# Kernel tuning notes

Measured on AMD Instinct MI355X. Metric: run time of the kernel, lower is better.

Reference implementation:

```python
import jax, jax.numpy as jnp
import numpy as np

N = 40000
E = 640000
F_IN = 128
F_OUT = 128


def setup_inputs() -> dict:
    key = jax.random.key(0)
    ks = jax.random.split(key, 8)
    x = jax.random.normal(ks[0], (N, F_IN), dtype=jnp.float32)
    weight = jax.random.normal(ks[1], (F_IN, F_OUT), dtype=jnp.float32) * (1.0 / np.sqrt(F_OUT))
    node_w = jax.random.normal(ks[2], (F_IN, 1), dtype=jnp.float32)
    sem_w = jax.random.normal(ks[3], (F_IN,), dtype=jnp.float32) * (1.0 / np.sqrt(F_IN))
    bias = jax.random.normal(ks[4], (F_OUT,), dtype=jnp.float32) * 0.01
    adj_val = jax.random.uniform(ks[5], (E,), dtype=jnp.float32)
    src = jax.random.randint(ks[6], (E,), 0, N, dtype=jnp.int32)
    dst = jax.random.randint(ks[7], (E,), 0, N, dtype=jnp.int32)
    return {"x": x, "weight": weight, "node_w": node_w, "sem_w": sem_w,
            "bias": bias, "adj_val": adj_val, "src": src, "dst": dst}


def reference(x, weight, node_w, sem_w, bias, adj_val, src, dst):
    # node-level attention: per-node sigmoid scalar [N, 1]
    node_att = jax.nn.sigmoid(x @ node_w)
    # semantic-level attention: softmax over feature weight vector [F_in]
    sem_att = jax.nn.softmax(sem_w)
    # hierarchical weighting, then dense projection [N, F_out]
    support = (x * node_att * sem_att) @ weight
    # spmm(adj, support): COO aggregation, row=dst, col=src
    msg = support[src] * adj_val[:, None]  # [E, F_out]
    out = jax.ops.segment_sum(msg, dst, num_segments=N)
    return out + bias
```

## Files before the change

kernel.cpp:

```cpp
#include <hip/hip_runtime.h>
#include <hip/hip_bf16.h>

#define F 128
#define ROWS 32
#define CAP 64

typedef unsigned long long u64;

__global__ __launch_bounds__(256, 4) void support_kernel(
    const float* __restrict__ x, const float* __restrict__ weight,
    const float* __restrict__ node_w, const float* __restrict__ sem_w,
    ushort4* __restrict__ support, int* __restrict__ cursor, int n_rows)
{
    __shared__ __align__(16) float xs[ROWS * F];
    __shared__ __align__(16) float sem[F];
    __shared__ float natt[ROWS];

    const int t = threadIdx.x;
    const int rbase = blockIdx.x * ROWS;

    if (cursor) {
        int gi = blockIdx.x * 256 + t;
        if (gi < n_rows) cursor[gi] = 0;
    }

    if (t < 64) {
        float v0 = sem_w[t], v1 = sem_w[t + 64];
        float m = fmaxf(v0, v1);
        #pragma unroll
        for (int off = 32; off; off >>= 1) m = fmaxf(m, __shfl_xor(m, off));
        float e0 = __expf(v0 - m), e1 = __expf(v1 - m);
        float ssum = e0 + e1;
        #pragma unroll
        for (int off = 32; off; off >>= 1) ssum += __shfl_xor(ssum, off);
        float inv = 1.0f / ssum;
        sem[t] = e0 * inv;
        sem[t + 64] = e1 * inv;
    }

    const int k4 = t & 31;
    float4 nw4 = ((const float4*)node_w)[k4];
    #pragma unroll
    for (int i = 0; i < 4; ++i) {
        int j = t + i * 256;
        int r = j >> 5;
        int gr = rbase + r;
        float4 v = make_float4(0.f, 0.f, 0.f, 0.f);
        if (gr < n_rows) v = ((const float4*)x)[(size_t)gr * 32 + k4];
        ((float4*)xs)[j] = v;
        float p = v.x * nw4.x + v.y * nw4.y + v.z * nw4.z + v.w * nw4.w;
        p += __shfl_xor(p, 1);  p += __shfl_xor(p, 2);  p += __shfl_xor(p, 4);
        p += __shfl_xor(p, 8);  p += __shfl_xor(p, 16);
        if ((t & 31) == 0) natt[r] = p;
    }
    __syncthreads();

    if (t < ROWS) {
        float z = natt[t];
        natt[t] = 1.0f / (1.0f + __expf(-z));
    }
    __syncthreads();

    #pragma unroll
    for (int i = 0; i < 4; ++i) {
        int j = t + i * 256;
        int r = j >> 5, kk = j & 31;
        float4 v = ((float4*)xs)[j];
        float4 s4 = ((float4*)sem)[kk];
        float a = natt[r];
        v.x *= a * s4.x; v.y *= a * s4.y; v.z *= a * s4.z; v.w *= a * s4.w;
        ((float4*)xs)[j] = v;
    }
    __syncthreads();

    const int cg = t & 31;
    const int rg = t >> 5;
    const float4* __restrict__ W4 = (const float4*)weight;
    float acc[4][4] = {};
    for (int k = 0; k < F; k += 4) {
        float4 w0 = W4[(k + 0) * 32 + cg];
        float4 w1 = W4[(k + 1) * 32 + cg];
        float4 w2 = W4[(k + 2) * 32 + cg];
        float4 w3 = W4[(k + 3) * 32 + cg];
        #pragma unroll
        for (int i = 0; i < 4; ++i) {
            float4 s = *(const float4*)&xs[(4 * rg + i) * F + k];
            acc[i][0] = fmaf(s.x, w0.x, acc[i][0]);
            acc[i][1] = fmaf(s.x, w0.y, acc[i][1]);
            acc[i][2] = fmaf(s.x, w0.z, acc[i][2]);
            acc[i][3] = fmaf(s.x, w0.w, acc[i][3]);
            acc[i][0] = fmaf(s.y, w1.x, acc[i][0]);
            acc[i][1] = fmaf(s.y, w1.y, acc[i][1]);
            acc[i][2] = fmaf(s.y, w1.z, acc[i][2]);
            acc[i][3] = fmaf(s.y, w1.w, acc[i][3]);
            acc[i][0] = fmaf(s.z, w2.x, acc[i][0]);
            acc[i][1] = fmaf(s.z, w2.y, acc[i][1]);
            acc[i][2] = fmaf(s.z, w2.z, acc[i][2]);
            acc[i][3] = fmaf(s.z, w2.w, acc[i][3]);
            acc[i][0] = fmaf(s.w, w3.x, acc[i][0]);
            acc[i][1] = fmaf(s.w, w3.y, acc[i][1]);
            acc[i][2] = fmaf(s.w, w3.z, acc[i][2]);
            acc[i][3] = fmaf(s.w, w3.w, acc[i][3]);
        }
    }

    #pragma unroll
    for (int i = 0; i < 4; ++i) {
        int r = rbase + 4 * rg + i;
        if (r < n_rows) {
            __hip_bfloat16 h0 = __float2bfloat16(acc[i][0]);
            __hip_bfloat16 h1 = __float2bfloat16(acc[i][1]);
            __hip_bfloat16 h2 = __float2bfloat16(acc[i][2]);
            __hip_bfloat16 h3 = __float2bfloat16(acc[i][3]);
            ushort4 o;
            o.x = *(unsigned short*)&h0;
            o.y = *(unsigned short*)&h1;
            o.z = *(unsigned short*)&h2;
            o.w = *(unsigned short*)&h3;
            support[(size_t)r * 32 + cg] = o;
        }
    }
}

__global__ void append_kernel(const int* __restrict__ dst, const int* __restrict__ src,
                              const float* __restrict__ adj_val,
                              int* __restrict__ cursor, int2* __restrict__ payload, int e) {
    int i = blockIdx.x * blockDim.x + threadIdx.x;
    if (i < e) {
        int d = dst[i];
        int s = atomicAdd(&cursor[d], 1);
        if (s < CAP)
            payload[(size_t)d * CAP + s] = make_int2(src[i], __float_as_int(adj_val[i]));
    }
}

__device__ __forceinline__ void bf16x4_fma(uint2 v, float a, float4& acc) {
    float f0 = __uint_as_float(v.x << 16);
    float f1 = __uint_as_float(v.x & 0xffff0000u);
    float f2 = __uint_as_float(v.y << 16);
    float f3 = __uint_as_float(v.y & 0xffff0000u);
    acc.x = fmaf(a, f0, acc.x);
    acc.y = fmaf(a, f1, acc.y);
    acc.z = fmaf(a, f2, acc.z);
    acc.w = fmaf(a, f3, acc.w);
}

__global__ __launch_bounds__(256) void aggregate_kernel(
    const uint2* __restrict__ support, const int* __restrict__ cursor,
    const int2* __restrict__ payload, const float* __restrict__ bias,
    float* __restrict__ out, int Nn)
{
    const int gw = (int)((blockIdx.x * (unsigned)blockDim.x + threadIdx.x) >> 6);
    const int lane = threadIdx.x & 63;
    const int half = lane >> 5;
    const int l32  = lane & 31;
    if (gw >= Nn) return;
    int deg = cursor[gw];
    deg = deg > CAP ? CAP : deg;
    const int2* __restrict__ pay = payload + (size_t)gw * CAP;

    float4 acc = make_float4(0.f, 0.f, 0.f, 0.f);
    int i = 0;
    for (; i + 8 <= deg; i += 8) {
        int2 p0 = pay[i + 0 + half];
        int2 p1 = pay[i + 2 + half];
        int2 p2 = pay[i + 4 + half];
        int2 p3 = pay[i + 6 + half];
        uint2 v0 = support[(size_t)p0.x * 32 + l32];
        uint2 v1 = support[(size_t)p1.x * 32 + l32];
        uint2 v2 = support[(size_t)p2.x * 32 + l32];
        uint2 v3 = support[(size_t)p3.x * 32 + l32];
        bf16x4_fma(v0, __int_as_float(p0.y), acc);
        bf16x4_fma(v1, __int_as_float(p1.y), acc);
        bf16x4_fma(v2, __int_as_float(p2.y), acc);
        bf16x4_fma(v3, __int_as_float(p3.y), acc);
    }
    for (; i + 2 <= deg; i += 2) {
        int2 p = pay[i + half];
        uint2 v = support[(size_t)p.x * 32 + l32];
        bf16x4_fma(v, __int_as_float(p.y), acc);
    }
    if (i < deg && half == 0) {
        int2 p = pay[i];
        uint2 v = support[(size_t)p.x * 32 + l32];
        bf16x4_fma(v, __int_as_float(p.y), acc);
    }

    acc.x += __shfl_xor(acc.x, 32);
    acc.y += __shfl_xor(acc.y, 32);
    acc.z += __shfl_xor(acc.z, 32);
    acc.w += __shfl_xor(acc.w, 32);

    if (half == 0) {
        float4 b = ((const float4*)bias)[l32];
        ((float4*)out)[(size_t)gw * 32 + l32] =
            make_float4(acc.x + b.x, acc.y + b.y, acc.z + b.z, acc.w + b.w);
    }
}

__global__ void init_out_kernel(float* __restrict__ out, const float* __restrict__ bias, int n) {
    int i = blockIdx.x * blockDim.x + threadIdx.x;
    if (i < n) out[i] = bias[i & (F - 1)];
}

__global__ void edge_atomic_kernel(const uint2* __restrict__ support,
                                   const int* __restrict__ src, const int* __restrict__ dst,
                                   const float* __restrict__ adj_val, float* __restrict__ out, int e) {
    long long g = (long long)blockIdx.x * blockDim.x + threadIdx.x;
    if (g >= (long long)e * 32) return;
    int ed = (int)(g >> 5), q = (int)(g & 31);
    float a = adj_val[ed];
    uint2 v = support[(size_t)src[ed] * 32 + q];
    float f0 = __uint_as_float(v.x << 16);
    float f1 = __uint_as_float(v.x & 0xffff0000u);
    float f2 = __uint_as_float(v.y << 16);
    float f3 = __uint_as_float(v.y & 0xffff0000u);
    float* o = out + (size_t)dst[ed] * F + 4 * q;
    atomicAdd(o + 0, a * f0);
    atomicAdd(o + 1, a * f1);
    atomicAdd(o + 2, a * f2);
    atomicAdd(o + 3, a * f3);
}

extern "C" void kernel_launch(void* const* d_in, const int* in_sizes, int n_in,
                              void* d_out, int out_size, void* d_ws, size_t ws_size,
                              hipStream_t stream) {
    const float* x       = (const float*)d_in[0];
    const float* weight  = (const float*)d_in[1];
    const float* node_w  = (const float*)d_in[2];
    const float* sem_w   = (const float*)d_in[3];
    const float* bias    = (const float*)d_in[4];
    const float* adj_val = (const float*)d_in[5];
    const int*   src     = (const int*)d_in[6];
    const int*   dst     = (const int*)d_in[7];
    float* out = (float*)d_out;

    const int Nn = in_sizes[0] / F;
    const int Ee = in_sizes[5];

    char* ws = (char*)d_ws;
    size_t off = 0;
    auto alloc = [&](size_t bytes) {
        void* p = ws + off;
        off = (off + bytes + 255) & ~(size_t)255;
        return p;
    };
    ushort4* support = (ushort4*)alloc((size_t)Nn * F * sizeof(unsigned short));
    size_t need_atomic = off;
    int*  cursor  = (int*)alloc((size_t)Nn * sizeof(int));
    int2* payload = (int2*)alloc((size_t)Nn * CAP * sizeof(int2));
    size_t need_full = off;

    const bool full = (ws_size >= need_full);

    support_kernel<<<(Nn + ROWS - 1) / ROWS, 256, 0, stream>>>(
        x, weight, node_w, sem_w, support, full ? cursor : nullptr, Nn);

    if (full) {
        append_kernel<<<(Ee + 255) / 256, 256, 0, stream>>>(dst, src, adj_val,
                                                            cursor, payload, Ee);
        long long waves = (long long)Nn;
        int blocks = (int)((waves * 64 + 255) / 256);
        aggregate_kernel<<<blocks, 256, 0, stream>>>(
            (const uint2*)support, cursor, payload, bias, out, Nn);
    } else if (ws_size >= need_atomic) {
        init_out_kernel<<<((size_t)Nn * F + 255) / 256, 256, 0, stream>>>(out, bias, Nn * F);
        long long tot = (long long)Ee * 32;
        edge_atomic_kernel<<<(unsigned)((tot + 255) / 256), 256, 0, stream>>>(
            (const uint2*)support, src, dst, adj_val, out, Ee);
    }
}
```

Measured before the change: 92.74 us.

## Fuse support projection and edge append into one heterogeneous launch

The support projection and the edge-append bucketing now run in a single kernel, with block ranges split between the two roles, so they execute concurrently instead of back-to-back. Cursor zeroing moves into a separate small kernel that runs first, since the append blocks need zeroed cursors before they start. The fusion is meant to overlap the compute-bound projection with the atomic-heavy scatter and remove one launch gap. In exchange it adds a zeroing launch, and the append blocks share the register and LDS budget of the projection kernel, which may limit their occupancy.

```diff
diff --git a/kernel.cpp b/kernel.cpp
--- a/kernel.cpp
+++ b/kernel.cpp
@@ -7,22 +7,39 @@
 
 typedef unsigned long long u64;
 
-__global__ __launch_bounds__(256, 4) void support_kernel(
+__global__ void zero_kernel(int* __restrict__ p, int n) {
+    int i = blockIdx.x * blockDim.x + threadIdx.x;
+    if (i < n) p[i] = 0;
+}
+
+__global__ __launch_bounds__(256, 4) void fused_kernel(
     const float* __restrict__ x, const float* __restrict__ weight,
     const float* __restrict__ node_w, const float* __restrict__ sem_w,
-    ushort4* __restrict__ support, int* __restrict__ cursor, int n_rows)
+    ushort4* __restrict__ support,
+    const int* __restrict__ dst, const int* __restrict__ src,
+    const float* __restrict__ adj_val,
+    int* __restrict__ cursor, int2* __restrict__ payload,
+    int n_rows, int e, int nSup)
 {
     __shared__ __align__(16) float xs[ROWS * F];
     __shared__ __align__(16) float sem[F];
     __shared__ float natt[ROWS];
 
     const int t = threadIdx.x;
+
+    if ((int)blockIdx.x >= nSup) {
+        int i = (blockIdx.x - nSup) * 256 + t;
+        if (i < e) {
+            int d = dst[i];
+            int s = atomicAdd(&cursor[d], 1);
+            if (s < CAP)
+                payload[(size_t)d * CAP + s] =
+                    make_int2(src[i], __float_as_int(adj_val[i]));
+        }
+        return;
+    }
+
     const int rbase = blockIdx.x * ROWS;
-
-    if (cursor) {
-        int gi = blockIdx.x * 256 + t;
-        if (gi < n_rows) cursor[gi] = 0;
-    }
 
     if (t < 64) {
         float v0 = sem_w[t], v1 = sem_w[t + 64];
@@ -122,18 +139,6 @@
     }
 }
 
-__global__ void append_kernel(const int* __restrict__ dst, const int* __restrict__ src,
-                              const float* __restrict__ adj_val,
-                              int* __restrict__ cursor, int2* __restrict__ payload, int e) {
-    int i = blockIdx.x * blockDim.x + threadIdx.x;
-    if (i < e) {
-        int d = dst[i];
-        int s = atomicAdd(&cursor[d], 1);
-        if (s < CAP)
-            payload[(size_t)d * CAP + s] = make_int2(src[i], __float_as_int(adj_val[i]));
-    }
-}
-
 __device__ __forceinline__ void bf16x4_fma(uint2 v, float a, float4& acc) {
     float f0 = __uint_as_float(v.x << 16);
     float f1 = __uint_as_float(v.x & 0xffff0000u);
@@ -253,17 +258,22 @@
 
     const bool full = (ws_size >= need_full);
 
-    support_kernel<<<(Nn + ROWS - 1) / ROWS, 256, 0, stream>>>(
-        x, weight, node_w, sem_w, support, full ? cursor : nullptr, Nn);
-
     if (full) {
-        append_kernel<<<(Ee + 255) / 256, 256, 0, stream>>>(dst, src, adj_val,
-                                                            cursor, payload, Ee);
+        const int nSup = (Nn + ROWS - 1) / ROWS;
+        const int nApp = (Ee + 255) / 256;
+        zero_kernel<<<(Nn + 255) / 256, 256, 0, stream>>>(cursor, Nn);
+        fused_kernel<<<nSup + nApp, 256, 0, stream>>>(
+            x, weight, node_w, sem_w, support, dst, src, adj_val,
+            cursor, payload, Nn, Ee, nSup);
         long long waves = (long long)Nn;
         int blocks = (int)((waves * 64 + 255) / 256);
         aggregate_kernel<<<blocks, 256, 0, stream>>>(
             (const uint2*)support, cursor, payload, bias, out, Nn);
     } else if (ws_size >= need_atomic) {
+        const int nSup = (Nn + ROWS - 1) / ROWS;
+        fused_kernel<<<nSup, 256, 0, stream>>>(
+            x, weight, node_w, sem_w, support, dst, src, adj_val,
+            nullptr, nullptr, Nn, 0, nSup);
         init_out_kernel<<<((size_t)Nn * F + 255) / 256, 256, 0, stream>>>(out, bias, Nn * F);
         long long tot = (long long)Ee * 32;
         edge_atomic_kernel<<<(unsigned)((tot + 255) / 256), 256, 0, stream>>>(
```

After: 93.52 us. About the same (+0.8%).

## Partition edge append by XCC-local destination slices with work-stealing chunk queues

Applied to the files above, without the earlier changes.

The append kernel now reads the XCC ID and walks eight destination-node slices, starting with the one matching its own XCC. Blocks pull edge chunks from a per-slice atomic queue and only append edges whose destination falls in the current slice. The goal is to keep each slice's cursor atomics and payload writes inside one XCC's L2 instead of bouncing them across dies. In exchange, every XCC rescans the whole dst array once per slice, adding queue atomics and __syncthreads barriers.

```diff
diff --git a/kernel.cpp b/kernel.cpp
--- a/kernel.cpp
+++ b/kernel.cpp
@@ -4,13 +4,16 @@
 #define F 128
 #define ROWS 32
 #define CAP 64
+#define NSLICE 8
+#define CHUNK 2048
 
 typedef unsigned long long u64;
 
 __global__ __launch_bounds__(256, 4) void support_kernel(
     const float* __restrict__ x, const float* __restrict__ weight,
     const float* __restrict__ node_w, const float* __restrict__ sem_w,
-    ushort4* __restrict__ support, int* __restrict__ cursor, int n_rows)
+    ushort4* __restrict__ support, int* __restrict__ cursor,
+    int* __restrict__ qhead, int n_rows)
 {
     __shared__ __align__(16) float xs[ROWS * F];
     __shared__ __align__(16) float sem[F];
@@ -22,6 +25,7 @@
     if (cursor) {
         int gi = blockIdx.x * 256 + t;
         if (gi < n_rows) cursor[gi] = 0;
+        if (blockIdx.x == 0 && t < NSLICE) qhead[t] = 0;
     }
 
     if (t < 64) {
@@ -122,15 +126,42 @@
     }
 }
 
-__global__ void append_kernel(const int* __restrict__ dst, const int* __restrict__ src,
-                              const float* __restrict__ adj_val,
-                              int* __restrict__ cursor, int2* __restrict__ payload, int e) {
-    int i = blockIdx.x * blockDim.x + threadIdx.x;
-    if (i < e) {
-        int d = dst[i];
-        int s = atomicAdd(&cursor[d], 1);
-        if (s < CAP)
-            payload[(size_t)d * CAP + s] = make_int2(src[i], __float_as_int(adj_val[i]));
+__global__ __launch_bounds__(256) void append_kernel(
+    const int* __restrict__ dst, const int* __restrict__ src,
+    const float* __restrict__ adj_val,
+    int* __restrict__ cursor, int* __restrict__ qhead,
+    int2* __restrict__ payload, int e, int nps, int nchunks)
+{
+    __shared__ int sc;
+    unsigned xcc;
+    asm volatile("s_getreg_b32 %0, hwreg(HW_REG_XCC_ID)" : "=s"(xcc));
+    xcc &= (NSLICE - 1);
+
+    for (int ss = 0; ss < NSLICE; ++ss) {
+        const int s  = (int)((xcc + ss) & (NSLICE - 1));
+        const int lo = s * nps;
+        const int hi = lo + nps;
+        while (true) {
+            if (threadIdx.x == 0) sc = atomicAdd(&qhead[s], 1);
+            __syncthreads();
+            const int c = sc;
+            __syncthreads();
+            if (c >= nchunks) break;
+            const int base = c * CHUNK;
+            #pragma unroll
+            for (int k = 0; k < CHUNK / 256; ++k) {
+                int i = base + k * 256 + (int)threadIdx.x;
+                if (i < e) {
+                    int d = dst[i];
+                    if (d >= lo && d < hi) {
+                        int sl = atomicAdd(&cursor[d], 1);
+                        if (sl < CAP)
+                            payload[(size_t)d * CAP + sl] =
+                                make_int2(src[i], __float_as_int(adj_val[i]));
+                    }
+                }
+            }
+        }
     }
 }
 
@@ -248,17 +279,21 @@
     ushort4* support = (ushort4*)alloc((size_t)Nn * F * sizeof(unsigned short));
     size_t need_atomic = off;
     int*  cursor  = (int*)alloc((size_t)Nn * sizeof(int));
+    int*  qhead   = (int*)alloc(NSLICE * sizeof(int));
     int2* payload = (int2*)alloc((size_t)Nn * CAP * sizeof(int2));
     size_t need_full = off;
 
     const bool full = (ws_size >= need_full);
 
     support_kernel<<<(Nn + ROWS - 1) / ROWS, 256, 0, stream>>>(
-        x, weight, node_w, sem_w, support, full ? cursor : nullptr, Nn);
+        x, weight, node_w, sem_w, support,
+        full ? cursor : nullptr, qhead, Nn);
 
     if (full) {
-        append_kernel<<<(Ee + 255) / 256, 256, 0, stream>>>(dst, src, adj_val,
-                                                            cursor, payload, Ee);
+        const int nps = (Nn + NSLICE - 1) / NSLICE;
+        const int nchunks = (Ee + CHUNK - 1) / CHUNK;
+        append_kernel<<<2048, 256, 0, stream>>>(
+            dst, src, adj_val, cursor, qhead, payload, Ee, nps, nchunks);
         long long waves = (long long)Nn;
         int blocks = (int)((waves * 64 + 255) / 256);
         aggregate_kernel<<<blocks, 256, 0, stream>>>(
```

New measurement: 298.0 us. +221.4%, slower.

## Replace per-node atomic append with binned multisplit and shared-memory counting sort

Applied to the files above, without the earlier changes.

Drops the per-destination global atomic cursor and padded payload. Edges are now split into bins of 160 destination nodes, staged in shared memory and flushed to per-bin global queues in chunks of 8. A second kernel reads each bin's queue, counting-sorts the edges by local node in shared memory, then aggregates bf16 support rows per node with one wave per node. The goal is fewer scattered global atomics and writes. In exchange, each bin queue is read four times (once per sub-block), padding records inflate the queues, and fixed capacities (QCAP, RAWCAP, OVCAP, 16-bit src and 8-bit local index packing) can silently drop edges on other input distributions.

```diff
diff --git a/kernel.cpp b/kernel.cpp
--- a/kernel.cpp
+++ b/kernel.cpp
@@ -3,14 +3,23 @@
 
 #define F 128
 #define ROWS 32
-#define CAP 64
+#define NPB 160
+#define NBIN_MAX 250
+#define NSUB 4
+#define SUBN (NPB / NSUB)
+#define STAGE_CAP 16
+#define QCAP 6144
+#define EPB 1280
+#define RAWCAP 1024
+#define OVCAP 4096
 
 typedef unsigned long long u64;
 
 __global__ __launch_bounds__(256, 4) void support_kernel(
     const float* __restrict__ x, const float* __restrict__ weight,
     const float* __restrict__ node_w, const float* __restrict__ sem_w,
-    ushort4* __restrict__ support, int* __restrict__ cursor, int n_rows)
+    ushort4* __restrict__ support, int* __restrict__ qhead,
+    int* __restrict__ ovcnt, int nbin, int n_rows)
 {
     __shared__ __align__(16) float xs[ROWS * F];
     __shared__ __align__(16) float sem[F];
@@ -19,9 +28,9 @@
     const int t = threadIdx.x;
     const int rbase = blockIdx.x * ROWS;
 
-    if (cursor) {
-        int gi = blockIdx.x * 256 + t;
-        if (gi < n_rows) cursor[gi] = 0;
+    if (qhead && blockIdx.x == 0) {
+        if (t < nbin) qhead[t] = 0;
+        if (t == 255) *ovcnt = 0;
     }
 
     if (t < 64) {
@@ -122,15 +131,66 @@
     }
 }
 
-__global__ void append_kernel(const int* __restrict__ dst, const int* __restrict__ src,
-                              const float* __restrict__ adj_val,
-                              int* __restrict__ cursor, int2* __restrict__ payload, int e) {
-    int i = blockIdx.x * blockDim.x + threadIdx.x;
-    if (i < e) {
-        int d = dst[i];
-        int s = atomicAdd(&cursor[d], 1);
-        if (s < CAP)
-            payload[(size_t)d * CAP + s] = make_int2(src[i], __float_as_int(adj_val[i]));
+__global__ __launch_bounds__(256) void multisplit_kernel(
+    const int* __restrict__ dst, const int* __restrict__ src,
+    const float* __restrict__ adj_val,
+    int* __restrict__ qhead, u64* __restrict__ queue,
+    u64* __restrict__ qov, int* __restrict__ ovcnt, int e, int nbin)
+{
+    __shared__ u64 stage[NBIN_MAX * STAGE_CAP];
+    __shared__ int fill[256];
+    const int t = threadIdx.x;
+    if (t < nbin) fill[t] = 0;
+    __syncthreads();
+
+    const int base = blockIdx.x * EPB;
+    for (int b = 0; b < EPB; b += 256) {
+        int i = base + b + t;
+        if (i < e) {
+            int d = dst[i];
+            int bin = d / NPB;
+            int dl = d - bin * NPB;
+            u64 rec = (u64)(unsigned)src[i]
+                    | ((u64)(unsigned)dl << 16)
+                    | ((u64)(unsigned)__float_as_int(adj_val[i]) << 32);
+            int sl = atomicAdd(&fill[bin], 1);
+            if (sl < STAGE_CAP) {
+                stage[bin * STAGE_CAP + sl] = rec;
+            } else {
+                u64 ovr = (u64)(unsigned)src[i]
+                        | ((u64)(unsigned)d << 16)
+                        | ((u64)(unsigned)__float_as_int(adj_val[i]) << 32);
+                int o = atomicAdd(ovcnt, 1);
+                if (o < OVCAP) qov[o] = ovr;
+            }
+        }
+        __syncthreads();
+        if (t < nbin) {
+            if (fill[t] > STAGE_CAP) fill[t] = STAGE_CAP;
+            while (fill[t] >= 8) {
+                int bq = atomicAdd(&qhead[t], 8);
+                if (bq + 8 <= QCAP) {
+                    u64* q = queue + (size_t)t * QCAP + bq;
+                    #pragma unroll
+                    for (int k = 0; k < 8; ++k) q[k] = stage[t * STAGE_CAP + k];
+                }
+                int f = fill[t];
+                for (int k = 8; k < f; ++k)
+                    stage[t * STAGE_CAP + k - 8] = stage[t * STAGE_CAP + k];
+                fill[t] = f - 8;
+            }
+        }
+        __syncthreads();
+    }
+    if (t < nbin && fill[t] > 0) {
+        int f = fill[t];
+        for (int k = f; k < 8; ++k) stage[t * STAGE_CAP + k] = (u64)0xFFull << 16;
+        int bq = atomicAdd(&qhead[t], 8);
+        if (bq + 8 <= QCAP) {
+            u64* q = queue + (size_t)t * QCAP + bq;
+            #pragma unroll
+            for (int k = 0; k < 8; ++k) q[k] = stage[t * STAGE_CAP + k];
+        }
     }
 }
 
@@ -145,56 +205,119 @@
     acc.w = fmaf(a, f3, acc.w);
 }
 
-__global__ __launch_bounds__(256) void aggregate_kernel(
-    const uint2* __restrict__ support, const int* __restrict__ cursor,
-    const int2* __restrict__ payload, const float* __restrict__ bias,
+__global__ __launch_bounds__(256) void binagg_kernel(
+    const u64* __restrict__ queue, const int* __restrict__ qhead,
+    const u64* __restrict__ qov, const int* __restrict__ ovcnt,
+    const uint2* __restrict__ support, const float* __restrict__ bias,
     float* __restrict__ out, int Nn)
 {
-    const int gw = (int)((blockIdx.x * (unsigned)blockDim.x + threadIdx.x) >> 6);
-    const int lane = threadIdx.x & 63;
+    __shared__ u64 raw[RAWCAP];
+    __shared__ u64 srt[RAWCAP];
+    __shared__ int cnt[SUBN], pre[SUBN + 1], cur[SUBN];
+    __shared__ int tot;
+
+    const int t = threadIdx.x;
+    const int bin = blockIdx.x / NSUB;
+    const int sub = blockIdx.x % NSUB;
+    const int node_lo = bin * NPB + sub * SUBN;
+    const int dl_lo = sub * SUBN;
+    const int nloc = min(SUBN, Nn - node_lo);
+    if (nloc <= 0) return;
+
+    if (t < SUBN) cnt[t] = 0;
+    if (t == 0) tot = 0;
+    __syncthreads();
+
+    int qlen = qhead[bin]; if (qlen > QCAP) qlen = QCAP;
+    const u64* __restrict__ q = queue + (size_t)bin * QCAP;
+    for (int i = t; i < qlen; i += 256) {
+        u64 r = q[i];
+        int ln = (int)((r >> 16) & 0xFF) - dl_lo;
+        if (ln >= 0 && ln < nloc) {
+            int s = atomicAdd(&tot, 1);
+            if (s < RAWCAP) {
+                raw[s] = (r & 0xFFFF) | ((u64)(unsigned)ln << 16)
+                       | (r & 0xFFFFFFFF00000000ull);
+                atomicAdd(&cnt[ln], 1);
+            }
+        }
+    }
+    int oc = *ovcnt; oc = oc < 0 ? 0 : (oc > OVCAP ? OVCAP : oc);
+    for (int i = t; i < oc; i += 256) {
+        u64 r = qov[i];
+        int ln = (int)((r >> 16) & 0xFFFF) - node_lo;
+        if (ln >= 0 && ln < nloc) {
+            int s = atomicAdd(&tot, 1);
+            if (s < RAWCAP) {
+                raw[s] = (r & 0xFFFF) | ((u64)(unsigned)ln << 16)
+                       | (r & 0xFFFFFFFF00000000ull);
+                atomicAdd(&cnt[ln], 1);
+            }
+        }
+    }
+    __syncthreads();
+
+    if (t == 0) {
+        int s = 0;
+        for (int j = 0; j < nloc; ++j) { pre[j] = s; s += cnt[j]; }
+        pre[nloc] = s;
+    }
+    __syncthreads();
+    if (t < nloc) cur[t] = pre[t];
+    __syncthreads();
+
+    int tstored = tot; if (tstored > RAWCAP) tstored = RAWCAP;
+    for (int i = t; i < tstored; i += 256) {
+        u64 r = raw[i];
+        int ln = (int)((r >> 16) & 0xFF);
+        int s = atomicAdd(&cur[ln], 1);
+        srt[s] = r;
+    }
+    __syncthreads();
+
+    const int wave = t >> 6;
+    const int lane = t & 63;
     const int half = lane >> 5;
     const int l32  = lane & 31;
-    if (gw >= Nn) return;
-    int deg = cursor[gw];
-    deg = deg > CAP ? CAP : deg;
-    const int2* __restrict__ pay = payload + (size_t)gw * CAP;
-
-    float4 acc = make_float4(0.f, 0.f, 0.f, 0.f);
-    int i = 0;
-    for (; i + 8 <= deg; i += 8) {
-        int2 p0 = pay[i + 0 + half];
-        int2 p1 = pay[i + 2 + half];
-        int2 p2 = pay[i + 4 + half];
-        int2 p3 = pay[i + 6 + half];
-        uint2 v0 = support[(size_t)p0.x * 32 + l32];
-        uint2 v1 = support[(size_t)p1.x * 32 + l32];
-        uint2 v2 = support[(size_t)p2.x * 32 + l32];
-        uint2 v3 = support[(size_t)p3.x * 32 + l32];
-        bf16x4_fma(v0, __int_as_float(p0.y), acc);
-        bf16x4_fma(v1, __int_as_float(p1.y), acc);
-        bf16x4_fma(v2, __int_as_float(p2.y), acc);
-        bf16x4_fma(v3, __int_as_float(p3.y), acc);
-    }
-    for (; i + 2 <= deg; i += 2) {
-        int2 p = pay[i + half];
-        uint2 v = support[(size_t)p.x * 32 + l32];
-        bf16x4_fma(v, __int_as_float(p.y), acc);
-    }
-    if (i < deg && half == 0) {
-        int2 p = pay[i];
-        uint2 v = support[(size_t)p.x * 32 + l32];
-        bf16x4_fma(v, __int_as_float(p.y), acc);
-    }
-
-    acc.x += __shfl_xor(acc.x, 32);
-    acc.y += __shfl_xor(acc.y, 32);
-    acc.z += __shfl_xor(acc.z, 32);
-    acc.w += __shfl_xor(acc.w, 32);
-
-    if (half == 0) {
-        float4 b = ((const float4*)bias)[l32];
-        ((float4*)out)[(size_t)gw * 32 + l32] =
-            make_float4(acc.x + b.x, acc.y + b.y, acc.z + b.z, acc.w + b.w);
+    for (int j = wave; j < nloc; j += 4) {
+        const int i0 = pre[j], i1 = pre[j + 1];
+        float4 acc = make_float4(0.f, 0.f, 0.f, 0.f);
+        int i = i0;
+        for (; i + 8 <= i1; i += 8) {
+            u64 r0 = srt[i + 0 + half];
+            u64 r1 = srt[i + 2 + half];
+            u64 r2 = srt[i + 4 + half];
+            u64 r3 = srt[i + 6 + half];
+            uint2 v0 = support[(size_t)(r0 & 0xFFFF) * 32 + l32];
+            uint2 v1 = support[(size_t)(r1 & 0xFFFF) * 32 + l32];
+            uint2 v2 = support[(size_t)(r2 & 0xFFFF) * 32 + l32];
+            uint2 v3 = support[(size_t)(r3 & 0xFFFF) * 32 + l32];
+            bf16x4_fma(v0, __int_as_float((int)(r0 >> 32)), acc);
+            bf16x4_fma(v1, __int_as_float((int)(r1 >> 32)), acc);
+            bf16x4_fma(v2, __int_as_float((int)(r2 >> 32)), acc);
+            bf16x4_fma(v3, __int_as_float((int)(r3 >> 32)), acc);
+        }
+        for (; i + 2 <= i1; i += 2) {
+            u64 r = srt[i + half];
+            uint2 v = support[(size_t)(r & 0xFFFF) * 32 + l32];
+            bf16x4_fma(v, __int_as_float((int)(r >> 32)), acc);
+        }
+        if (i < i1 && half == 0) {
+            u64 r = srt[i];
+            uint2 v = support[(size_t)(r & 0xFFFF) * 32 + l32];
+            bf16x4_fma(v, __int_as_float((int)(r >> 32)), acc);
+        }
+
+        acc.x += __shfl_xor(acc.x, 32);
+        acc.y += __shfl_xor(acc.y, 32);
+        acc.z += __shfl_xor(acc.z, 32);
+        acc.w += __shfl_xor(acc.w, 32);
+
+        if (half == 0) {
+            float4 b = ((const float4*)bias)[l32];
+            ((float4*)out)[(size_t)(node_lo + j) * 32 + l32] =
+                make_float4(acc.x + b.x, acc.y + b.y, acc.z + b.z, acc.w + b.w);
+        }
     }
 }
 
@@ -208,14 +331,14 @@
                                    const float* __restrict__ adj_val, float* __restrict__ out, int e) {
     long long g = (long long)blockIdx.x * blockDim.x + threadIdx.x;
     if (g >= (long long)e * 32) return;
-    int ed = (int)(g >> 5), q = (int)(g & 31);
+    int ed = (int)(g >> 5), qq = (int)(g & 31);
     float a = adj_val[ed];
-    uint2 v = support[(size_t)src[ed] * 32 + q];
+    uint2 v = support[(size_t)src[ed] * 32 + qq];
     float f0 = __uint_as_float(v.x << 16);
     float f1 = __uint_as_float(v.x & 0xffff0000u);
     float f2 = __uint_as_float(v.y << 16);
     float f3 = __uint_as_float(v.y & 0xffff0000u);
-    float* o = out + (size_t)dst[ed] * F + 4 * q;
+    float* o = out + (size_t)dst[ed] * F + 4 * qq;
     atomicAdd(o + 0, a * f0);
     atomicAdd(o + 1, a * f1);
     atomicAdd(o + 2, a * f2);
@@ -247,22 +370,25 @@
     };
     ushort4* support = (ushort4*)alloc((size_t)Nn * F * sizeof(unsigned short));
     size_t need_atomic = off;
-    int*  cursor  = (int*)alloc((size_t)Nn * sizeof(int));
-    int2* payload = (int2*)alloc((size_t)Nn * CAP * sizeof(int2));
+    const int nbin = (Nn + NPB - 1) / NPB;
+    int*  qhead = (int*)alloc((size_t)nbin * sizeof(int));
+    int*  ovcnt = (int*)alloc(256 * sizeof(int));
+    u64*  qov   = (u64*)alloc((size_t)OVCAP * sizeof(u64));
+    u64*  queue = (u64*)alloc((size_t)nbin * QCAP * sizeof(u64));
     size_t need_full = off;
 
-    const bool full = (ws_size >= need_full);
+    const bool full = (ws_size >= need_full) && (Nn <= 65536) && (nbin <= NBIN_MAX);
 
     support_kernel<<<(Nn + ROWS - 1) / ROWS, 256, 0, stream>>>(
-        x, weight, node_w, sem_w, support, full ? cursor : nullptr, Nn);
+        x, weight, node_w, sem_w, support,
+        full ? qhead : nullptr, ovcnt, nbin, Nn);
 
     if (full) {
-        append_kernel<<<(Ee + 255) / 256, 256, 0, stream>>>(dst, src, adj_val,
-                                                            cursor, payload, Ee);
-        long long waves = (long long)Nn;
-        int blocks = (int)((waves * 64 + 255) / 256);
-        aggregate_kernel<<<blocks, 256, 0, stream>>>(
-            (const uint2*)support, cursor, payload, bias, out, Nn);
+        const int msblocks = (Ee + EPB - 1) / EPB;
+        multisplit_kernel<<<msblocks, 256, 0, stream>>>(
+            dst, src, adj_val, qhead, queue, qov, ovcnt, Ee, nbin);
+        binagg_kernel<<<nbin * NSUB, 256, 0, stream>>>(
+            queue, qhead, qov, ovcnt, (const uint2*)support, bias, out, Nn);
     } else if (ws_size >= need_atomic) {
         init_out_kernel<<<((size_t)Nn * F + 255) / 256, 256, 0, stream>>>(out, bias, Nn * F);
         long long tot = (long long)Ee * 32;
```

Measured after the change: 96.38 us. +3.9%, slower.
